# Optimization experiments

Hardware: AMD Instinct MI355X
Metric: run time of the kernel (lower is better)

Reference implementation:

```python
import jax, jax.numpy as jnp
import numpy as np

B, H, W, C = 16, 256, 256, 16
HO, WO = 256, 256


def setup_inputs() -> dict:
    key = jax.random.key(0)
    k1, k2 = jax.random.split(key)
    x = jax.random.normal(k1, (B, H, W, C), dtype=jnp.float32)
    # loc network: global avg pool -> dense(C, 6); small weights, identity bias
    W_loc = jax.random.normal(k2, (C, 6), dtype=jnp.float32) * 0.01
    b_loc = jnp.asarray([1.0, 0.0, 0.0, 1.0, 0.0, 0.0], dtype=jnp.float32)
    # coords_grid = np.indices(output_grid_shape): (2, HO, WO), [0]=row idx, [1]=col idx
    coords_grid = jnp.asarray(np.indices((HO, WO), dtype=np.float32))
    return {"x": x, "W_loc": W_loc, "b_loc": b_loc, "coords_grid": coords_grid}


def _forward(x, W_loc, b_loc, coords_grid):
    # loc network: predict 6 affine params per batch element
    pooled = jnp.mean(x, axis=(1, 2))              # [B, C]
    params = pooled @ W_loc + b_loc                # [B, 6]
    A = params[:, :4].reshape(-1, 2, 2)            # [B, 2, 2]
    t = params[:, 4:]                              # [B, 2]
    # grid_transform_fn: affine map of pixel coordinates
    tc = jnp.einsum('bij,jhw->bihw', A, coords_grid) + t[:, :, None, None]  # [B,2,HO,WO]
    yc, xc = tc[:, 0], tc[:, 1]                    # [B, HO, WO] each
    # interpolation_fn: bilinear sampling with clipping (wrap=False)
    y0 = jnp.floor(yc)
    x0 = jnp.floor(xc)
    wy = yc - y0                                   # fractional weights
    wx = xc - x0
    y0i = jnp.clip(y0.astype(jnp.int32), 0, H - 1)
    y1i = jnp.clip(y0.astype(jnp.int32) + 1, 0, H - 1)
    x0i = jnp.clip(x0.astype(jnp.int32), 0, W - 1)
    x1i = jnp.clip(x0.astype(jnp.int32) + 1, 0, W - 1)
    bidx = jnp.arange(x.shape[0])[:, None, None]   # [B,1,1] batch gather index
    Ia = x[bidx, y0i, x0i]                         # [B,HO,WO,C]
    Ib = x[bidx, y0i, x1i]
    Ic = x[bidx, y1i, x0i]
    Id = x[bidx, y1i, x1i]
    wa = ((1.0 - wy) * (1.0 - wx))[..., None]
    wb = ((1.0 - wy) * wx)[..., None]
    wc = (wy * (1.0 - wx))[..., None]
    wd = (wy * wx)[..., None]
    return wa * Ia + wb * Ib + wc * Ic + wd * Id   # [B,HO,WO,C]


def reference(x, W_loc, b_loc, coords_grid):
    return _forward(x, W_loc, b_loc, coords_grid)
```

## Files before the change

kernel.cpp:

```cpp
#include <hip/hip_runtime.h>

#define BB 16
#define HH 256
#define WW 256
#define CC 16
#define NPIX (HH * WW)
#define SLICES 128
#define POOL_BLOCKS (BB * SLICES)
#define SAMPLE_BPB 128
#define SAMPLE_BLOCKS (BB * SAMPLE_BPB)

__global__ __launch_bounds__(256) void pool_partial(const float4* __restrict__ x4,
                                                    float4* __restrict__ part) {
    const int blk = blockIdx.x;
    const int tid = threadIdx.x;
    const float4* p = x4 + (size_t)blk * 2048 + tid;
    float4 acc = {0.f, 0.f, 0.f, 0.f};
#pragma unroll
    for (int k = 0; k < 8; ++k) {
        float4 v = p[k * 256];
        acc.x += v.x; acc.y += v.y; acc.z += v.z; acc.w += v.w;
    }
    for (int off = 4; off < 64; off <<= 1) {
        acc.x += __shfl_down(acc.x, off);
        acc.y += __shfl_down(acc.y, off);
        acc.z += __shfl_down(acc.z, off);
        acc.w += __shfl_down(acc.w, off);
    }
    __shared__ float4 wsum[4][4];
    const int wave = tid >> 6, lane = tid & 63;
    if (lane < 4) wsum[wave][lane] = acc;
    __syncthreads();
    if (tid < 4) {
        float4 t0 = wsum[0][tid], t1 = wsum[1][tid];
        float4 t2 = wsum[2][tid], t3 = wsum[3][tid];
        float4 t;
        t.x = t0.x + t1.x + t2.x + t3.x;
        t.y = t0.y + t1.y + t2.y + t3.y;
        t.z = t0.z + t1.z + t2.z + t3.z;
        t.w = t0.w + t1.w + t2.w + t3.w;
        part[blk * 4 + tid] = t;
    }
}

__global__ __launch_bounds__(256) void sample_fused(
    const float4* __restrict__ x4,
    const float* __restrict__ W_loc,
    const float* __restrict__ b_loc,
    const float4* __restrict__ part,
    float4* __restrict__ out)
{
    const int tid  = threadIdx.x;
    const int blk  = blockIdx.x;
    const int b    = blk >> 7;
    const int wave = tid >> 6, lane = tid & 63;

    __shared__ float4 wsum[4][4];
    __shared__ float  pooled[CC];
    __shared__ float  pr[6];

    {
        const float4* q = part + (size_t)b * 512;
        float4 a0 = q[tid], a1 = q[tid + 256];
        float4 acc;
        acc.x = a0.x + a1.x; acc.y = a0.y + a1.y;
        acc.z = a0.z + a1.z; acc.w = a0.w + a1.w;
        for (int off = 4; off < 64; off <<= 1) {
            acc.x += __shfl_down(acc.x, off);
            acc.y += __shfl_down(acc.y, off);
            acc.z += __shfl_down(acc.z, off);
            acc.w += __shfl_down(acc.w, off);
        }
        if (lane < 4) wsum[wave][lane] = acc;
        __syncthreads();
        if (tid < 4) {
            float4 t0 = wsum[0][tid], t1 = wsum[1][tid];
            float4 t2 = wsum[2][tid], t3 = wsum[3][tid];
            pooled[tid * 4 + 0] = (t0.x + t1.x + t2.x + t3.x) * (1.0f / 65536.0f);
            pooled[tid * 4 + 1] = (t0.y + t1.y + t2.y + t3.y) * (1.0f / 65536.0f);
            pooled[tid * 4 + 2] = (t0.z + t1.z + t2.z + t3.z) * (1.0f / 65536.0f);
            pooled[tid * 4 + 3] = (t0.w + t1.w + t2.w + t3.w) * (1.0f / 65536.0f);
        }
        __syncthreads();
        if (tid < 6) {
            float a = b_loc[tid];
#pragma unroll
            for (int c = 0; c < CC; ++c)
                a += pooled[c] * W_loc[c * 6 + tid];
            pr[tid] = a;
        }
        __syncthreads();
    }

    const float p0 = pr[0], p1 = pr[1], p2 = pr[2];
    const float p3 = pr[3], p4 = pr[4], p5 = pr[5];
    const size_t base    = (size_t)b * NPIX;
    const int    pixBase = (blk & 127) * 512 + (tid >> 2);
    const int    cq      = tid & 3;

#pragma unroll 4
    for (int k = 0; k < 8; ++k) {
        const int pix = pixBase + k * 64;
        const int h = pix >> 8;
        const int w = pix & 255;

        const float fh = (float)h, fw = (float)w;
        const float yc = p0 * fh + p1 * fw + p4;
        const float xc = p2 * fh + p3 * fw + p5;

        const float y0f = floorf(yc), x0f = floorf(xc);
        const float wy = yc - y0f, wx = xc - x0f;
        const int y0 = (int)y0f, x0 = (int)x0f;
        const int y0i = min(max(y0, 0), HH - 1);
        const int y1i = min(max(y0 + 1, 0), HH - 1);
        const int x0i = min(max(x0, 0), WW - 1);
        const int x1i = min(max(x0 + 1, 0), WW - 1);

        const float4* r0 = x4 + (base + (size_t)y0i * WW) * 4 + cq;
        const float4* r1 = x4 + (base + (size_t)y1i * WW) * 4 + cq;
        const float4 Ia = r0[(size_t)x0i * 4];
        const float4 Ib = r0[(size_t)x1i * 4];
        const float4 Ic = r1[(size_t)x0i * 4];
        const float4 Id = r1[(size_t)x1i * 4];

        const float wa = (1.f - wy) * (1.f - wx);
        const float wb = (1.f - wy) * wx;
        const float wc = wy * (1.f - wx);
        const float wd = wy * wx;

        float4 o;
        o.x = wa * Ia.x + wb * Ib.x + wc * Ic.x + wd * Id.x;
        o.y = wa * Ia.y + wb * Ib.y + wc * Ic.y + wd * Id.y;
        o.z = wa * Ia.z + wb * Ib.z + wc * Ic.z + wd * Id.z;
        o.w = wa * Ia.w + wb * Ib.w + wc * Ic.w + wd * Id.w;

        out[(base + pix) * 4 + cq] = o;
    }
}

extern "C" void kernel_launch(void* const* d_in, const int* in_sizes, int n_in,
                              void* d_out, int out_size, void* d_ws, size_t ws_size,
                              hipStream_t stream) {
    const float* x     = (const float*)d_in[0];
    const float* W_loc = (const float*)d_in[1];
    const float* b_loc = (const float*)d_in[2];

    float4* part = (float4*)d_ws;

    pool_partial<<<POOL_BLOCKS, 256, 0, stream>>>((const float4*)x, part);
    sample_fused<<<SAMPLE_BLOCKS, 256, 0, stream>>>((const float4*)x, W_loc, b_loc,
                                                    part, (float4*)d_out);
}
```

Measured before the change: 129.7 us.

## Split affine param computation into separate kernel; use 32-bit byte offsets and nontemporal stores

```diff
diff --git a/kernel.cpp b/kernel.cpp
--- a/kernel.cpp
+++ b/kernel.cpp
@@ -7,8 +7,9 @@
 #define NPIX (HH * WW)
 #define SLICES 128
 #define POOL_BLOCKS (BB * SLICES)
-#define SAMPLE_BPB 128
-#define SAMPLE_BLOCKS (BB * SAMPLE_BPB)
+#define SAMPLE_BLOCKS (BB * 128)
+
+typedef float vf4 __attribute__((ext_vector_type(4)));
 
 __global__ __launch_bounds__(256) void pool_partial(const float4* __restrict__ x4,
                                                     float4* __restrict__ part) {
@@ -43,98 +44,101 @@
     }
 }
 
-__global__ __launch_bounds__(256) void sample_fused(
-    const float4* __restrict__ x4,
-    const float* __restrict__ W_loc,
-    const float* __restrict__ b_loc,
-    const float4* __restrict__ part,
-    float4* __restrict__ out)
-{
-    const int tid  = threadIdx.x;
-    const int blk  = blockIdx.x;
-    const int b    = blk >> 7;
+__global__ __launch_bounds__(256) void params_kernel(const float4* __restrict__ part,
+                                                     const float* __restrict__ W_loc,
+                                                     const float* __restrict__ b_loc,
+                                                     float* __restrict__ prm) {
+    const int b   = blockIdx.x;
+    const int tid = threadIdx.x;
     const int wave = tid >> 6, lane = tid & 63;
-
     __shared__ float4 wsum[4][4];
     __shared__ float  pooled[CC];
-    __shared__ float  pr[6];
 
-    {
-        const float4* q = part + (size_t)b * 512;
-        float4 a0 = q[tid], a1 = q[tid + 256];
-        float4 acc;
-        acc.x = a0.x + a1.x; acc.y = a0.y + a1.y;
-        acc.z = a0.z + a1.z; acc.w = a0.w + a1.w;
-        for (int off = 4; off < 64; off <<= 1) {
-            acc.x += __shfl_down(acc.x, off);
-            acc.y += __shfl_down(acc.y, off);
-            acc.z += __shfl_down(acc.z, off);
-            acc.w += __shfl_down(acc.w, off);
-        }
-        if (lane < 4) wsum[wave][lane] = acc;
-        __syncthreads();
-        if (tid < 4) {
-            float4 t0 = wsum[0][tid], t1 = wsum[1][tid];
-            float4 t2 = wsum[2][tid], t3 = wsum[3][tid];
-            pooled[tid * 4 + 0] = (t0.x + t1.x + t2.x + t3.x) * (1.0f / 65536.0f);
-            pooled[tid * 4 + 1] = (t0.y + t1.y + t2.y + t3.y) * (1.0f / 65536.0f);
-            pooled[tid * 4 + 2] = (t0.z + t1.z + t2.z + t3.z) * (1.0f / 65536.0f);
-            pooled[tid * 4 + 3] = (t0.w + t1.w + t2.w + t3.w) * (1.0f / 65536.0f);
-        }
-        __syncthreads();
-        if (tid < 6) {
-            float a = b_loc[tid];
+    const float4* q = part + (size_t)b * 512;
+    float4 a0 = q[tid], a1 = q[tid + 256];
+    float4 acc;
+    acc.x = a0.x + a1.x; acc.y = a0.y + a1.y;
+    acc.z = a0.z + a1.z; acc.w = a0.w + a1.w;
+    for (int off = 4; off < 64; off <<= 1) {
+        acc.x += __shfl_down(acc.x, off);
+        acc.y += __shfl_down(acc.y, off);
+        acc.z += __shfl_down(acc.z, off);
+        acc.w += __shfl_down(acc.w, off);
+    }
+    if (lane < 4) wsum[wave][lane] = acc;
+    __syncthreads();
+    if (tid < 4) {
+        float4 t0 = wsum[0][tid], t1 = wsum[1][tid];
+        float4 t2 = wsum[2][tid], t3 = wsum[3][tid];
+        pooled[tid * 4 + 0] = (t0.x + t1.x + t2.x + t3.x) * (1.0f / 65536.0f);
+        pooled[tid * 4 + 1] = (t0.y + t1.y + t2.y + t3.y) * (1.0f / 65536.0f);
+        pooled[tid * 4 + 2] = (t0.z + t1.z + t2.z + t3.z) * (1.0f / 65536.0f);
+        pooled[tid * 4 + 3] = (t0.w + t1.w + t2.w + t3.w) * (1.0f / 65536.0f);
+    }
+    __syncthreads();
+    if (tid < 6) {
+        float a = b_loc[tid];
 #pragma unroll
-            for (int c = 0; c < CC; ++c)
-                a += pooled[c] * W_loc[c * 6 + tid];
-            pr[tid] = a;
-        }
-        __syncthreads();
+        for (int c = 0; c < CC; ++c)
+            a += pooled[c] * W_loc[c * 6 + tid];
+        prm[b * 8 + tid] = a;
     }
+}
 
-    const float p0 = pr[0], p1 = pr[1], p2 = pr[2];
-    const float p3 = pr[3], p4 = pr[4], p5 = pr[5];
-    const size_t base    = (size_t)b * NPIX;
-    const int    pixBase = (blk & 127) * 512 + (tid >> 2);
-    const int    cq      = tid & 3;
+__global__ __launch_bounds__(256) void sample_v2(const char* __restrict__ xb0,
+                                                 const float* __restrict__ prm,
+                                                 char* __restrict__ ob0) {
+    const int tid = threadIdx.x;
+    const int blk = blockIdx.x;
+    const int b   = blk >> 7;
+
+    const float* pp = prm + b * 8;
+    const float p0 = pp[0], p1 = pp[1], p2 = pp[2];
+    const float p3 = pp[3], p4 = pp[4], p5 = pp[5];
+
+    const char* xb = xb0 + ((size_t)b << 22);
+    char*       ob = ob0 + ((size_t)b << 22);
+    const unsigned int cqo = (unsigned int)(tid & 3) << 4;
+
+    const int pixBase = (blk & 127) * 512 + (tid >> 2);
+    const int h0 = (blk & 127) * 2;
+    const int w0 = tid >> 2;
 
 #pragma unroll 4
     for (int k = 0; k < 8; ++k) {
-        const int pix = pixBase + k * 64;
-        const int h = pix >> 8;
-        const int w = pix & 255;
+        const int hh  = h0 + (k >> 2);
+        const int wpx = w0 + ((k & 3) << 6);
 
-        const float fh = (float)h, fw = (float)w;
+        const float fh = (float)hh, fw = (float)wpx;
         const float yc = p0 * fh + p1 * fw + p4;
         const float xc = p2 * fh + p3 * fw + p5;
 
         const float y0f = floorf(yc), x0f = floorf(xc);
         const float wy = yc - y0f, wx = xc - x0f;
-        const int y0 = (int)y0f, x0 = (int)x0f;
-        const int y0i = min(max(y0, 0), HH - 1);
+        const int y0 = (int)y0f, x0v = (int)x0f;
+        const int y0i = min(max(y0,     0), HH - 1);
         const int y1i = min(max(y0 + 1, 0), HH - 1);
-        const int x0i = min(max(x0, 0), WW - 1);
-        const int x1i = min(max(x0 + 1, 0), WW - 1);
+        const int x0i = min(max(x0v,     0), WW - 1);
+        const int x1i = min(max(x0v + 1, 0), WW - 1);
 
-        const float4* r0 = x4 + (base + (size_t)y0i * WW) * 4 + cq;
-        const float4* r1 = x4 + (base + (size_t)y1i * WW) * 4 + cq;
-        const float4 Ia = r0[(size_t)x0i * 4];
-        const float4 Ib = r0[(size_t)x1i * 4];
-        const float4 Ic = r1[(size_t)x0i * 4];
-        const float4 Id = r1[(size_t)x1i * 4];
+        const unsigned int r0 = ((unsigned int)y0i << 14) + cqo;
+        const unsigned int r1 = ((unsigned int)y1i << 14) + cqo;
+        const unsigned int c0 = (unsigned int)x0i << 6;
+        const unsigned int c1 = (unsigned int)x1i << 6;
 
-        const float wa = (1.f - wy) * (1.f - wx);
-        const float wb = (1.f - wy) * wx;
-        const float wc = wy * (1.f - wx);
-        const float wd = wy * wx;
+        const vf4 Ia = *(const vf4*)(xb + (r0 + c0));
+        const vf4 Ib = *(const vf4*)(xb + (r0 + c1));
+        const vf4 Ic = *(const vf4*)(xb + (r1 + c0));
+        const vf4 Id = *(const vf4*)(xb + (r1 + c1));
 
-        float4 o;
-        o.x = wa * Ia.x + wb * Ib.x + wc * Ic.x + wd * Id.x;
-        o.y = wa * Ia.y + wb * Ib.y + wc * Ic.y + wd * Id.y;
-        o.z = wa * Ia.z + wb * Ib.z + wc * Ic.z + wd * Id.z;
-        o.w = wa * Ia.w + wb * Ib.w + wc * Ic.w + wd * Id.w;
+        const float omy = 1.f - wy, omx = 1.f - wx;
+        const float wa = omy * omx, wb_ = omy * wx;
+        const float wc_ = wy * omx, wd = wy * wx;
 
-        out[(base + pix) * 4 + cq] = o;
+        vf4 o = wa * Ia + wb_ * Ib + wc_ * Ic + wd * Id;
+
+        const unsigned int po = ((unsigned int)(pixBase + (k << 6)) << 6) + cqo;
+        __builtin_nontemporal_store(o, (vf4*)(ob + po));
     }
 }
 
@@ -146,8 +150,9 @@
     const float* b_loc = (const float*)d_in[2];
 
     float4* part = (float4*)d_ws;
+    float*  prm  = (float*)((char*)d_ws + 2048 * 4 * sizeof(float4));
 
     pool_partial<<<POOL_BLOCKS, 256, 0, stream>>>((const float4*)x, part);
-    sample_fused<<<SAMPLE_BLOCKS, 256, 0, stream>>>((const float4*)x, W_loc, b_loc,
-                                                    part, (float4*)d_out);
+    params_kernel<<<BB, 256, 0, stream>>>(part, W_loc, b_loc, prm);
+    sample_v2<<<SAMPLE_BLOCKS, 256, 0, stream>>>((const char*)x, prm, (char*)d_out);
 }
```

Measured after the change: 133.4 us. 1.03x slower.
